# Kernel optimization log

Measured on AMD Instinct MI355X. Metric: run time of the kernel, lower is better.

The kernel has to match this reference:

```python
import jax, jax.numpy as jnp
import numpy as np

N, D, HID, E, XD = 50000, 128, 64, 800000, 3

def _p(key, shape, scale=0.05):
    return jax.random.normal(key, shape, dtype=jnp.float32) * scale

def setup_inputs() -> dict:
    key = jax.random.key(0)
    ks = jax.random.split(key, 16)
    h = jax.random.normal(ks[0], (N, D), dtype=jnp.float32)
    x = jax.random.normal(ks[1], (N, XD), dtype=jnp.float32)
    edge_index = jax.random.randint(ks[2], (2, E), 0, N, dtype=jnp.int32)
    return {
        'h': h, 'x': x, 'edge_index': edge_index,
        'We1': _p(ks[3], (HID, 2 * D + 1)), 'be1': jnp.zeros((HID,), jnp.float32),
        'We2': _p(ks[4], (HID, HID)), 'be2': jnp.zeros((HID,), jnp.float32),
        'ln_g': jnp.ones((HID,), jnp.float32), 'ln_b': jnp.zeros((HID,), jnp.float32),
        'Wh1': _p(ks[5], (HID, D + HID)), 'bh1': jnp.zeros((HID,), jnp.float32),
        'Wh2': _p(ks[6], (D, HID)), 'bh2': jnp.zeros((D,), jnp.float32),
        'Wx': _p(ks[7], (1, HID)), 'bx': jnp.zeros((1,), jnp.float32),
        'Wg': _p(ks[8], (1, HID)), 'bg': jnp.zeros((1,), jnp.float32),
    }

def reference(h, x, edge_index, We1, be1, We2, be2, ln_g, ln_b,
              Wh1, bh1, Wh2, bh2, Wx, bx, Wg, bg):
    src, dst = edge_index[0], edge_index[1]
    n_nodes = h.shape[0]
    r = x[src] - x[dst]                          # (E, 3)
    d_sq = jnp.sum(r * r, axis=-1, keepdims=True)  # (E, 1)
    r_n = r / (jnp.sqrt(d_sq) + 1e-8)
    # phi_e: Linear -> SiLU -> Linear -> SiLU -> LayerNorm
    e_in = jnp.concatenate([h[src], h[dst], d_sq], axis=-1)  # (E, 2d+1)
    z = jax.nn.silu(e_in @ We1.T + be1)
    z = jax.nn.silu(z @ We2.T + be2)
    mu = jnp.mean(z, axis=-1, keepdims=True)
    var = jnp.mean((z - mu) ** 2, axis=-1, keepdims=True)
    m = (z - mu) * jax.lax.rsqrt(var + 1e-5) * ln_g + ln_b   # (E, hid)
    # gate and gated messages
    alpha = jax.nn.sigmoid(m @ Wg.T + bg)                     # (E, 1)
    m_gated = m * alpha
    agg_h = jax.ops.segment_sum(m_gated, dst, num_segments=n_nodes)  # (N, hid)
    # coordinate update (tanh_coords=True)
    cw = jnp.tanh(m_gated @ Wx.T + bx)                        # (E, 1)
    agg_x = jax.ops.segment_sum(r_n * cw, dst, num_segments=n_nodes)  # (N, 3)
    # coords_agg='mean': divide by in-degree clamped to 1
    deg = jax.ops.segment_sum(jnp.ones((src.shape[0], 1), h.dtype), dst,
                              num_segments=n_nodes)
    agg_x = agg_x / jnp.maximum(deg, 1.0)
    # phi_h residual update
    hh = jax.nn.silu(jnp.concatenate([h, agg_h], axis=-1) @ Wh1.T + bh1)
    h_new = h + (hh @ Wh2.T + bh2)
    x_new = x + agg_x
    return (h_new, x_new)
```

## Files before the change

### kernel.cpp

```cpp
#include <hip/hip_runtime.h>
#include <math.h>

#define HID 64
#define DF  128
#define HB  256

typedef __attribute__((ext_vector_type(8))) short short8v;
typedef __attribute__((ext_vector_type(4))) float float4v;
typedef __attribute__((ext_vector_type(4))) unsigned int uint4v;

__device__ __forceinline__ float silu_f(float v) {
    return v * __builtin_amdgcn_rcpf(1.0f + __expf(-v));
}

__device__ __forceinline__ unsigned short f2bf(float f) {
    unsigned u = __float_as_uint(f);
    u += 0x7FFFu + ((u >> 16) & 1u);
    return (unsigned short)(u >> 16);
}

__device__ __forceinline__ unsigned cvt2(float lo, float hi) {
    unsigned r;
    asm("v_cvt_pk_bf16_f32 %0, %1, %2" : "=v"(r) : "v"(lo), "v"(hi));
    return r;
}

__device__ __forceinline__ short8v pack8(float a0, float a1, float a2, float a3,
                                         float a4, float a5, float a6, float a7) {
    uint4v w;
    w[0] = cvt2(a0, a1);
    w[1] = cvt2(a2, a3);
    w[2] = cvt2(a4, a5);
    w[3] = cvt2(a6, a7);
    union { uint4v u; short8v s; } cv;
    cv.u = w;
    return cv.s;
}

__device__ __forceinline__ short8v pack_bf16(float4 a, float4 b) {
    return pack8(a.x, a.y, a.z, a.w, b.x, b.y, b.z, b.w);
}

__device__ __forceinline__ void wredsum4(float& a, float& b, float& c, float& d) {
#pragma unroll
    for (int t = 1; t < 64; t <<= 1) {
        a += __shfl_xor(a, t, 64);
        b += __shfl_xor(b, t, 64);
        c += __shfl_xor(c, t, 64);
        d += __shfl_xor(d, t, 64);
    }
}

#define PREPW 61504
__global__ void prep_weights(const float* __restrict__ We1, const float* __restrict__ We2,
                             const float* __restrict__ Wh1, const float* __restrict__ Wh2,
                             float* __restrict__ Wt1, float* __restrict__ Wt2,
                             unsigned short* __restrict__ WbfA,
                             unsigned short* __restrict__ WpB1,
                             unsigned short* __restrict__ WpH1,
                             unsigned short* __restrict__ WpH2,
                             int* __restrict__ cnt, int N) {
    int i = blockIdx.x * 256 + threadIdx.x;
    if (i >= PREPW) {
        int n = i - PREPW;
        if (n < N) cnt[n] = 0;
        return;
    }
    if (i < 257 * 64) {
        int k = i >> 6, f = i & 63;
        Wt1[i] = We1[f * 257 + k];
        return;
    }
    int j = i - 257 * 64;
    if (j < 64 * 64) {
        int k = j >> 6, f = j & 63;
        Wt2[j] = We2[f * 64 + k];
        return;
    }
    j -= 64 * 64;
    if (j < 4096) {
        int jj = j & 7, lane = (j >> 3) & 63, kc = (j >> 9) & 1, t = (j >> 10) & 3;
        int f = t * 16 + (lane & 15);
        int k = kc * 32 + ((lane >> 4) * 8) + jj;
        WbfA[j] = f2bf(We2[f * 64 + k]);
        return;
    }
    j -= 4096;
    if (j < 16384) {
        int jj = j & 7, lane = (j >> 3) & 63, kc = (j >> 9) & 3, ft = j >> 11;
        int f = ft * 16 + (lane & 15);
        int k = kc * 32 + ((lane >> 4) * 8) + jj;
        float v = (f < 64) ? We1[f * 257 + k] : We1[(f - 64) * 257 + 128 + k];
        WpB1[j] = f2bf(v);
        return;
    }
    j -= 16384;
    if (j < 12288) {
        int jj = j & 7, lane = (j >> 3) & 63, idx = j >> 9;
        int kc = idx % 6, ft = idx / 6;
        int f = ft * 16 + (lane & 15);
        int k = kc * 32 + ((lane >> 4) * 8) + jj;
        WpH1[j] = f2bf(Wh1[f * 192 + k]);
        return;
    }
    j -= 12288;
    if (j < 8192) {
        int jj = j & 7, lane = (j >> 3) & 63, idx = j >> 9;
        int kc = idx & 1, ft = idx >> 1;
        int c = ft * 16 + (lane & 15);
        int k = kc * 32 + ((lane >> 4) * 8) + jj;
        WpH2[j] = f2bf(Wh2[c * 64 + k]);
        return;
    }
}

__global__ __launch_bounds__(256) void count_kernel(const int* __restrict__ dst,
                                                    int* __restrict__ cnt,
                                                    int* __restrict__ rank, int E) {
    int e = blockIdx.x * 256 + threadIdx.x;
    if (e >= E) return;
    int r = atomicAdd(&cnt[dst[e]], 1);
    if (rank) rank[e] = r;
}

__global__ __launch_bounds__(1024) void scan1(const int* __restrict__ cnt,
                                              int* __restrict__ off,
                                              int* __restrict__ bsum, int N) {
    __shared__ int sm[1024];
    int tid = threadIdx.x;
    int i = blockIdx.x * 1024 + tid;
    int v = (i < N) ? cnt[i] : 0;
    sm[tid] = v;
    __syncthreads();
    for (int ofs = 1; ofs < 1024; ofs <<= 1) {
        int t = (tid >= ofs) ? sm[tid - ofs] : 0;
        __syncthreads();
        sm[tid] += t;
        __syncthreads();
    }
    if (i < N) off[i] = sm[tid] - v;
    if (tid == 1023) bsum[blockIdx.x] = sm[1023];
}

__global__ __launch_bounds__(256) void scan3(int* __restrict__ off,
                                             const int* __restrict__ bsum,
                                             int Nb, int N, int E) {
    __shared__ int pref[64];
    if (threadIdx.x == 0) {
        int s = 0;
        for (int b = 0; b < Nb; ++b) { pref[b] = s; s += bsum[b]; }
    }
    __syncthreads();
    int i = blockIdx.x * 256 + threadIdx.x;
    if (i > N) return;
    if (i == N) off[N] = E;
    else off[i] += pref[i >> 10];
}

__global__ __launch_bounds__(256) void scatter_src(const int* __restrict__ dst,
                                                   const int* __restrict__ srcI,
                                                   const int* __restrict__ rank,
                                                   const int* __restrict__ off,
                                                   int* __restrict__ csr_src, int E) {
    int e = blockIdx.x * 256 + threadIdx.x;
    if (e >= E) return;
    csr_src[off[dst[e]] + rank[e]] = srcI[e];
}

__global__ __launch_bounds__(HB) void hist_local(const int* __restrict__ cnt,
                                                 int* __restrict__ lrank,
                                                 int* __restrict__ blockcnt, int N) {
    __shared__ int lh[64];
    int tid = threadIdx.x;
    if (tid < 64) lh[tid] = 0;
    __syncthreads();
    int n = blockIdx.x * HB + tid;
    if (n < N) {
        int b = min(cnt[n], 63);
        lrank[n] = atomicAdd(&lh[b], 1);
    }
    __syncthreads();
    if (tid < 64) blockcnt[blockIdx.x * 64 + tid] = lh[tid];
}

__global__ __launch_bounds__(1024) void hist_tot(const int* __restrict__ blockcnt,
                                                 int* __restrict__ bucketbase, int nblk) {
    __shared__ int part[16][64];
    int b = threadIdx.x & 63, j = threadIdx.x >> 6;
    int s = 0;
    for (int k = j; k < nblk; k += 16) s += blockcnt[k * 64 + b];
    part[j][b] = s;
    __syncthreads();
    if (threadIdx.x < 64) {
        int t = 0;
#pragma unroll
        for (int jj = 1; jj < 16; ++jj) t += part[jj][threadIdx.x];
        part[0][threadIdx.x] += t;
    }
    __syncthreads();
    if (threadIdx.x == 0) {
        int base = 0;
        for (int bb = 0; bb < 64; ++bb) {
            int t = part[0][bb];
            bucketbase[bb] = base;
            base += t;
        }
    }
}

__global__ __launch_bounds__(64) void hist_scan2(int* __restrict__ blockcnt,
                                                 const int* __restrict__ bucketbase,
                                                 int nblk) {
    int b = blockIdx.x;
    int lane = threadIdx.x;
    int carry = bucketbase[b];
    for (int chunk = 0; chunk * 64 < nblk; ++chunk) {
        int k = chunk * 64 + lane;
        int c = (k < nblk) ? blockcnt[k * 64 + b] : 0;
        int v = c;
#pragma unroll
        for (int ofs = 1; ofs < 64; ofs <<= 1) {
            int t = __shfl_up(v, ofs, 64);
            if (lane >= ofs) v += t;
        }
        if (k < nblk) blockcnt[k * 64 + b] = carry + v - c;
        carry += __shfl(v, 63, 64);
    }
}

__global__ __launch_bounds__(HB) void degscatter2(const int* __restrict__ cnt,
                                                  const int* __restrict__ lrank,
                                                  const int* __restrict__ blockcnt,
                                                  int* __restrict__ nodeorder, int N) {
    int n = blockIdx.x * HB + threadIdx.x;
    if (n >= N) return;
    int b = min(cnt[n], 63);
    int pos = blockcnt[(n / HB) * 64 + b] + lrank[n];
    nodeorder[N - 1 - pos] = n;
}

__global__ __launch_bounds__(256) void node_pre(
    const float* __restrict__ h, const unsigned short* __restrict__ WpB1,
    const float* __restrict__ be1, const float* __restrict__ xin,
    float* __restrict__ Ps, float* __restrict__ Pd,
    float4* __restrict__ x4, int N) {
    const int lane = threadIdx.x & 63;
    const int wslot = threadIdx.x >> 6;
    {
        int n = blockIdx.x * 64 + threadIdx.x;
        if (threadIdx.x < 64 && n < N)
            x4[n] = make_float4(xin[3 * n], xin[3 * n + 1], xin[3 * n + 2], 0.f);
    }
    const int tile = (blockIdx.x * 4 + wslot) * 16;
    if (tile >= N) return;
    const int r15 = lane & 15, kg = lane >> 4;
    const int arow = min(tile + r15, N - 1);
    const float* hr = h + (size_t)arow * DF + kg * 8;
    short8v A[4];
#pragma unroll
    for (int kc = 0; kc < 4; ++kc) {
        float4 q0 = *(const float4*)(hr + kc * 32);
        float4 q1 = *(const float4*)(hr + kc * 32 + 4);
        A[kc] = pack_bf16(q0, q1);
    }
#pragma unroll
    for (int ft = 0; ft < 8; ++ft) {
        float4v c = (float4v){0.f, 0.f, 0.f, 0.f};
#pragma unroll
        for (int kc = 0; kc < 4; ++kc) {
            short8v B = *(const short8v*)&WpB1[(((ft * 4 + kc) * 64) + lane) * 8];
            c = __builtin_amdgcn_mfma_f32_16x16x32_bf16(A[kc], B, c, 0, 0, 0);
        }
        int f = ft * 16 + r15;
        float bias = (f >= 64) ? be1[f - 64] : 0.f;
#pragma unroll
        for (int r = 0; r < 4; ++r) {
            int n = tile + kg * 4 + r;
            if (n < N) {
                float v = c[r] + bias;
                if (f < 64) Ps[(size_t)n * 64 + f] = v;
                else        Pd[(size_t)n * 64 + (f - 64)] = v;
            }
        }
    }
}

__global__ __launch_bounds__(256) void gather_kernel(
    const int* __restrict__ csr_src, const int* __restrict__ off,
    const int* __restrict__ nodeorder, const float4* __restrict__ x4,
    const float* __restrict__ Ps, const float* __restrict__ Pd,
    const float* __restrict__ Wt1, const unsigned short* __restrict__ WbfA,
    const float* __restrict__ be2,
    const float* __restrict__ ln_g, const float* __restrict__ ln_b,
    const float* __restrict__ Wx, const float* __restrict__ bx,
    const float* __restrict__ Wg, const float* __restrict__ bg,
    float* __restrict__ agg_h, float* __restrict__ xout, int N) {
    const int lane = threadIdx.x & 63;
    const int wid = blockIdx.x * 4 + (threadIdx.x >> 6);
    const int e16 = lane & 15;
    const int hg = lane >> 4;
    const int k0 = hg * 8;
    const int p = e16 & 3;
    if (wid * 4 >= N) return;
    const int slot = wid * 4 + (e16 >> 2);

    short8v a[4][2];
#pragma unroll
    for (int t = 0; t < 4; ++t)
#pragma unroll
        for (int kc = 0; kc < 2; ++kc)
            a[t][kc] = *(const short8v*)&WbfA[(((t * 2 + kc) * 64) + lane) * 8];

    const float* colW = Wt1 + 256 * HID;
    float colWk[16];
#pragma unroll
    for (int j = 0; j < 8; ++j) {
        colWk[j] = colW[k0 + j];
        colWk[8 + j] = colW[k0 + 32 + j];
    }
    float be2r[16], cgr[16], cxr[16];
#pragma unroll
    for (int t = 0; t < 4; ++t)
#pragma unroll
        for (int r = 0; r < 4; ++r) {
            int f = t * 16 + hg * 4 + r;
            float g = ln_g[f];
            be2r[4 * t + r] = be2[f];
            cgr[4 * t + r] = g * Wg[f];
            cxr[4 * t + r] = g * Wx[f];
        }
    const float bgs = bg[0], bxs = bx[0];

    float Cg = ln_g[lane] * Wg[lane], Cx = ln_g[lane] * Wx[lane];
    float Cbg = ln_b[lane] * Wg[lane], Cbx = ln_b[lane] * Wx[lane];
    wredsum4(Cg, Cx, Cbg, Cbx);
    const float g0 = (lane < 16) ? 1.0f : 0.0f;

    const int nj = (slot < N) ? nodeorder[slot] : -1;
    int beg = 0, end = 0;
    if (nj >= 0) { beg = off[nj]; end = off[nj + 1]; }
    const float4 xdv = (nj >= 0) ? x4[nj] : make_float4(0.f, 0.f, 0.f, 0.f);
    float baseK[16];
    {
        const float4v* pd4 = (const float4v*)(Pd + (size_t)max(nj, 0) * HID + k0);
        float4v p0 = pd4[0], p1 = pd4[1], p2 = pd4[8], p3 = pd4[9];
#pragma unroll
        for (int j = 0; j < 4; ++j) {
            baseK[j] = p0[j];
            baseK[4 + j] = p1[j];
            baseK[8 + j] = p2[j];
            baseK[12 + j] = p3[j];
        }
    }

    int nb = (end - beg + 3) >> 2;
#pragma unroll
    for (int mk = 1; mk < 64; mk <<= 1) nb = max(nb, __shfl_xor(nb, mk, 64));
    nb = __builtin_amdgcn_readfirstlane(nb);

    float4v acc[4];
#pragma unroll
    for (int t = 0; t < 4; ++t) acc[t] = (float4v){0.f, 0.f, 0.f, 0.f};
    float ax0 = 0.f, ax1 = 0.f, ax2 = 0.f, Sa = 0.f, Smu = 0.f;

    float4 xsC = xdv;
    float4v q0C = (float4v){0.f, 0.f, 0.f, 0.f}, q1C = q0C, q2C = q0C, q3C = q0C;
    if (nb > 0) {
        int idx = beg + p;
        int ic = (idx < end) ? idx : (end > 0 ? end - 1 : 0);
        int s0 = csr_src[ic];
        xsC = x4[s0];
        const float4v* ps4 = (const float4v*)(Ps + (size_t)s0 * HID + k0);
        q0C = ps4[0]; q1C = ps4[1]; q2C = ps4[8]; q3C = ps4[9];
    }

    for (int b = 0; b < nb; ++b) {
        float4 xs = xsC;
        float4v q0 = q0C, q1 = q1C, q2 = q2C, q3 = q3C;
        float validf = ((beg + b * 4 + p) < end) ? 1.0f : 0.0f;

        if (b + 1 < nb) {
            int idx2 = beg + (b + 1) * 4 + p;
            int ic2 = (idx2 < end) ? idx2 : (end > 0 ? end - 1 : 0);
            int sN = csr_src[ic2];
            xsC = x4[sN];
            const float4v* ps4 = (const float4v*)(Ps + (size_t)sN * HID + k0);
            q0C = ps4[0]; q1C = ps4[1]; q2C = ps4[8]; q3C = ps4[9];
        }

        float r0 = xs.x - xdv.x, r1 = xs.y - xdv.y, r2 = xs.z - xdv.z;
        float dsq = r0 * r0 + r1 * r1 + r2 * r2;
        float inv = __builtin_amdgcn_rcpf(__builtin_amdgcn_sqrtf(dsq) + 1e-8f);

        float zb[16];
#pragma unroll
        for (int j = 0; j < 4; ++j) {
            zb[j]      = silu_f(q0[j] + baseK[j] + dsq * colWk[j]);
            zb[4 + j]  = silu_f(q1[j] + baseK[4 + j] + dsq * colWk[4 + j]);
            zb[8 + j]  = silu_f(q2[j] + baseK[8 + j] + dsq * colWk[8 + j]);
            zb[12 + j] = silu_f(q3[j] + baseK[12 + j] + dsq * colWk[12 + j]);
        }
        short8v b0 = pack8(zb[0], zb[1], zb[2], zb[3], zb[4], zb[5], zb[6], zb[7]);
        short8v b1 = pack8(zb[8], zb[9], zb[10], zb[11], zb[12], zb[13], zb[14], zb[15]);

        float ms[16];
        float S1 = 0.f, S2 = 0.f, Sg = 0.f, Sx = 0.f;
#pragma unroll
        for (int t = 0; t < 4; ++t) {
            float4v c = (float4v){be2r[4 * t], be2r[4 * t + 1],
                                  be2r[4 * t + 2], be2r[4 * t + 3]};
            c = __builtin_amdgcn_mfma_f32_16x16x32_bf16(a[t][0], b0, c, 0, 0, 0);
            c = __builtin_amdgcn_mfma_f32_16x16x32_bf16(a[t][1], b1, c, 0, 0, 0);
#pragma unroll
            for (int r = 0; r < 4; ++r) {
                float v = c[r] * __builtin_amdgcn_rcpf(1.0f + __expf(-c[r]));
                ms[4 * t + r] = v;
                S1 += v;
                S2 = fmaf(v, v, S2);
                Sg = fmaf(v, cgr[4 * t + r], Sg);
                Sx = fmaf(v, cxr[4 * t + r], Sx);
            }
        }
#pragma unroll
        for (int mk = 16; mk < 64; mk <<= 1) {
            S1 += __shfl_xor(S1, mk, 64);
            S2 += __shfl_xor(S2, mk, 64);
            Sg += __shfl_xor(Sg, mk, 64);
            Sx += __shfl_xor(Sx, mk, 64);
        }

        float mu = S1 * (1.0f / HID);
        float var = S2 * (1.0f / HID) - mu * mu;
        float rstd = __builtin_amdgcn_rsqf(var + 1e-5f);
        float dg = fmaf(rstd, Sg - mu * Cg, Cbg);
        float dx = fmaf(rstd, Sx - mu * Cx, Cbx);
        float alpha = __builtin_amdgcn_rcpf(1.0f + __expf(-(dg + bgs))) * validf;
        float ta = __expf(2.0f * fmaf(alpha, dx, bxs));
        float cwv = 1.0f - 2.0f * __builtin_amdgcn_rcpf(ta + 1.0f);

        float u = rstd * alpha;
        Sa += alpha;
        Smu = fmaf(u, mu, Smu);
#pragma unroll
        for (int t = 0; t < 4; ++t) {
            float4v av = acc[t];
#pragma unroll
            for (int r = 0; r < 4; ++r) av[r] = fmaf(u, ms[4 * t + r], av[r]);
            acc[t] = av;
        }
        float rc = inv * cwv * validf * g0;
        ax0 = fmaf(r0, rc, ax0);
        ax1 = fmaf(r1, rc, ax1);
        ax2 = fmaf(r2, rc, ax2);
    }

#pragma unroll
    for (int t = 0; t < 4; ++t) {
        float4v av = acc[t];
#pragma unroll
        for (int r = 0; r < 4; ++r) {
            float v = av[r];
            v += __shfl_xor(v, 1, 64);
            v += __shfl_xor(v, 2, 64);
            av[r] = v;
        }
        acc[t] = av;
    }
    Sa  += __shfl_xor(Sa, 1, 64);  Sa  += __shfl_xor(Sa, 2, 64);
    Smu += __shfl_xor(Smu, 1, 64); Smu += __shfl_xor(Smu, 2, 64);
    ax0 += __shfl_xor(ax0, 1, 64); ax0 += __shfl_xor(ax0, 2, 64);
    ax1 += __shfl_xor(ax1, 1, 64); ax1 += __shfl_xor(ax1, 2, 64);
    ax2 += __shfl_xor(ax2, 1, 64); ax2 += __shfl_xor(ax2, 2, 64);

    if (p == 0 && nj >= 0) {
        float* dstp = agg_h + (size_t)nj * HID + hg * 4;
#pragma unroll
        for (int t = 0; t < 4; ++t) {
            int f = t * 16 + hg * 4;
            float4 o;
            o.x = fmaf(ln_g[f + 0], acc[t][0] - Smu, ln_b[f + 0] * Sa);
            o.y = fmaf(ln_g[f + 1], acc[t][1] - Smu, ln_b[f + 1] * Sa);
            o.z = fmaf(ln_g[f + 2], acc[t][2] - Smu, ln_b[f + 2] * Sa);
            o.w = fmaf(ln_g[f + 3], acc[t][3] - Smu, ln_b[f + 3] * Sa);
            *(float4*)(dstp + t * 16) = o;
        }
        if (hg == 0) {
            float invd = 1.0f / fmaxf((float)(end - beg), 1.0f);
            float* ox = xout + (size_t)nj * 3;
            ox[0] = xdv.x + ax0 * invd;
            ox[1] = xdv.y + ax1 * invd;
            ox[2] = xdv.z + ax2 * invd;
        }
    }
}

__global__ __launch_bounds__(256) void edge_kernel_atomic(
    const int* __restrict__ src, const int* __restrict__ dst,
    const float* __restrict__ x,
    const float* __restrict__ Ps, const float* __restrict__ Pd,
    const float* __restrict__ Wt1, const float* __restrict__ Wt2,
    const float* __restrict__ be2,
    const float* __restrict__ ln_g, const float* __restrict__ ln_b,
    const float* __restrict__ Wx, const float* __restrict__ bx,
    const float* __restrict__ Wg, const float* __restrict__ bg,
    float* __restrict__ agg_h, float* __restrict__ agg_x, int E) {
    int e = blockIdx.x * 256 + threadIdx.x;
    if (e >= E) return;
    int s = src[e], d = dst[e];
    float r0 = x[s * 3] - x[d * 3], r1 = x[s * 3 + 1] - x[d * 3 + 1], r2 = x[s * 3 + 2] - x[d * 3 + 2];
    float dsq = r0 * r0 + r1 * r1 + r2 * r2;
    float inv = 1.0f / (sqrtf(dsq) + 1e-8f);
    float rn0 = r0 * inv, rn1 = r1 * inv, rn2 = r2 * inv;
    float z[HID];
    const float4* ps = (const float4*)(Ps + (size_t)s * HID);
    const float4* pd = (const float4*)(Pd + (size_t)d * HID);
    const float* colW = Wt1 + 256 * HID;
#pragma unroll
    for (int f4 = 0; f4 < HID / 4; ++f4) {
        float4 aa = ps[f4];
        float4 b = pd[f4];
        float av[4] = {aa.x, aa.y, aa.z, aa.w};
        float bv[4] = {b.x, b.y, b.z, b.w};
#pragma unroll
        for (int j = 0; j < 4; ++j) {
            int f = 4 * f4 + j;
            z[f] = silu_f(av[j] + bv[j] + dsq * colW[f]);
        }
    }
    float m[HID];
#pragma unroll
    for (int f = 0; f < HID; ++f) m[f] = be2[f];
#pragma unroll
    for (int k = 0; k < HID; ++k) {
        float zv = z[k];
#pragma unroll
        for (int f = 0; f < HID; ++f) m[f] = fmaf(zv, Wt2[k * HID + f], m[f]);
    }
#pragma unroll
    for (int f = 0; f < HID; ++f) m[f] = silu_f(m[f]);
    float mu = 0.f;
#pragma unroll
    for (int f = 0; f < HID; ++f) mu += m[f];
    mu *= (1.0f / HID);
    float var = 0.f;
#pragma unroll
    for (int f = 0; f < HID; ++f) {
        float t = m[f] - mu;
        var = fmaf(t, t, var);
    }
    var *= (1.0f / HID);
    float rstd = 1.0f / sqrtf(var + 1e-5f);
#pragma unroll
    for (int f = 0; f < HID; ++f) m[f] = (m[f] - mu) * rstd * ln_g[f] + ln_b[f];
    float dotg = 0.f, dotx = 0.f;
#pragma unroll
    for (int f = 0; f < HID; ++f) {
        dotg = fmaf(m[f], Wg[f], dotg);
        dotx = fmaf(m[f], Wx[f], dotx);
    }
    float alpha = 1.0f / (1.0f + __expf(-(dotg + bg[0])));
    float ta = __expf(2.0f * fmaf(alpha, dotx, bx[0]));
    float cw = 1.0f - 2.0f / (ta + 1.0f);
    float* ah = agg_h + (size_t)d * HID;
#pragma unroll
    for (int f = 0; f < HID; ++f) atomicAdd(&ah[f], m[f] * alpha);
    atomicAdd(&agg_x[d * 3 + 0], rn0 * cw);
    atomicAdd(&agg_x[d * 3 + 1], rn1 * cw);
    atomicAdd(&agg_x[d * 3 + 2], rn2 * cw);
}

__global__ __launch_bounds__(256) void node_kernel(
    const float* __restrict__ h, const float* __restrict__ xin,
    const float* __restrict__ agg_h, const float* __restrict__ agg_x,
    const int* __restrict__ degI,
    const unsigned short* __restrict__ WpH1, const unsigned short* __restrict__ WpH2,
    const float* __restrict__ bh1, const float* __restrict__ bh2,
    float* __restrict__ out, int N, int writeX) {
    __shared__ float hhL[4][16][72];
    const int lane = threadIdx.x & 63;
    const int wslot = threadIdx.x >> 6;
    if (writeX) {
        int n = blockIdx.x * 64 + threadIdx.x;
        if (threadIdx.x < 64 && n < N) {
            float dv = (float)degI[n];
            float invd = 1.0f / fmaxf(dv, 1.0f);
            float* ox = out + (size_t)N * DF + (size_t)n * 3;
            ox[0] = xin[n * 3 + 0] + agg_x[n * 3 + 0] * invd;
            ox[1] = xin[n * 3 + 1] + agg_x[n * 3 + 1] * invd;
            ox[2] = xin[n * 3 + 2] + agg_x[n * 3 + 2] * invd;
        }
    }
    const int tile = (blockIdx.x * 4 + wslot) * 16;
    if (tile >= N) return;
    const int r15 = lane & 15, kg = lane >> 4;
    const int arow = min(tile + r15, N - 1);

    short8v A[6];
    const float* hr = h + (size_t)arow * DF + kg * 8;
#pragma unroll
    for (int kc = 0; kc < 4; ++kc) {
        float4 q0 = *(const float4*)(hr + kc * 32);
        float4 q1 = *(const float4*)(hr + kc * 32 + 4);
        A[kc] = pack_bf16(q0, q1);
    }
    const float* ar = agg_h + (size_t)arow * HID + kg * 8;
#pragma unroll
    for (int kc = 0; kc < 2; ++kc) {
        float4 q0 = *(const float4*)(ar + kc * 32);
        float4 q1 = *(const float4*)(ar + kc * 32 + 4);
        A[4 + kc] = pack_bf16(q0, q1);
    }

#pragma unroll
    for (int ft = 0; ft < 4; ++ft) {
        float4v c = (float4v){0.f, 0.f, 0.f, 0.f};
#pragma unroll
        for (int kc = 0; kc < 6; ++kc) {
            short8v B = *(const short8v*)&WpH1[(((ft * 6 + kc) * 64) + lane) * 8];
            c = __builtin_amdgcn_mfma_f32_16x16x32_bf16(A[kc], B, c, 0, 0, 0);
        }
        int f = ft * 16 + r15;
        float b1v = bh1[f];
#pragma unroll
        for (int r = 0; r < 4; ++r)
            hhL[wslot][kg * 4 + r][f] = silu_f(c[r] + b1v);
    }
    __builtin_amdgcn_wave_barrier();

    short8v HA[2];
#pragma unroll
    for (int kc = 0; kc < 2; ++kc) {
        float4 q0 = *(const float4*)&hhL[wslot][r15][kc * 32 + kg * 8];
        float4 q1 = *(const float4*)&hhL[wslot][r15][kc * 32 + kg * 8 + 4];
        HA[kc] = pack_bf16(q0, q1);
    }

#pragma unroll
    for (int ft = 0; ft < 8; ++ft) {
        float4v c = (float4v){0.f, 0.f, 0.f, 0.f};
#pragma unroll
        for (int kc = 0; kc < 2; ++kc) {
            short8v B = *(const short8v*)&WpH2[(((ft * 2 + kc) * 64) + lane) * 8];
            c = __builtin_amdgcn_mfma_f32_16x16x32_bf16(HA[kc], B, c, 0, 0, 0);
        }
        int cc = ft * 16 + r15;
        float b2 = bh2[cc];
#pragma unroll
        for (int r = 0; r < 4; ++r) {
            int n = tile + kg * 4 + r;
            if (n < N)
                out[(size_t)n * DF + cc] = h[(size_t)n * DF + cc] + c[r] + b2;
        }
    }
}

extern "C" void kernel_launch(void* const* d_in, const int* in_sizes, int n_in,
                              void* d_out, int out_size, void* d_ws, size_t ws_size,
                              hipStream_t stream) {
    const float* h    = (const float*)d_in[0];
    const float* x    = (const float*)d_in[1];
    const int*   ei   = (const int*)d_in[2];
    const float* We1  = (const float*)d_in[3];
    const float* be1  = (const float*)d_in[4];
    const float* We2  = (const float*)d_in[5];
    const float* be2  = (const float*)d_in[6];
    const float* ln_g = (const float*)d_in[7];
    const float* ln_b = (const float*)d_in[8];
    const float* Wh1  = (const float*)d_in[9];
    const float* bh1  = (const float*)d_in[10];
    const float* Wh2  = (const float*)d_in[11];
    const float* bh2  = (const float*)d_in[12];
    const float* Wx   = (const float*)d_in[13];
    const float* bx   = (const float*)d_in[14];
    const float* Wg   = (const float*)d_in[15];
    const float* bg   = (const float*)d_in[16];

    const int E = in_sizes[2] / 2;
    const int N = in_sizes[0] / DF;
    const int* src = ei;
    const int* dst = ei + E;

    char* base = (char*)d_ws;
    size_t o = 0;
    auto carve = [&](size_t bytes) -> void* {
        void* r = base + o;
        o = (o + bytes + 15) & ~(size_t)15;
        return r;
    };
    const int nblk = (N + HB - 1) / HB;
    float* agg_h = (float*)carve((size_t)N * HID * 4);
    float* agg_x = (float*)carve((size_t)N * 3 * 4);
    float* Wt1   = (float*)carve(257 * 64 * 4);
    float* Wt2   = (float*)carve(64 * 64 * 4);
    unsigned short* WbfA = (unsigned short*)carve(4096 * 2);
    unsigned short* WpB1 = (unsigned short*)carve(16384 * 2);
    unsigned short* WpH1 = (unsigned short*)carve(12288 * 2);
    unsigned short* WpH2 = (unsigned short*)carve(8192 * 2);
    int*   cnt   = (int*)carve((size_t)N * 4);
    int*   off   = (int*)carve(((size_t)N + 1) * 4);
    int*   bsum  = (int*)carve(256 * 4);
    int*   lrank = (int*)carve((size_t)N * 4);
    int*   blockcnt = (int*)carve((size_t)nblk * 64 * 4);
    int*   bucketbase = (int*)carve(64 * 4);
    int*   nodeorder = (int*)carve((size_t)N * 4);
    float4* x4   = (float4*)carve((size_t)N * 16);
    int*   rank  = (int*)carve((size_t)E * 4);
    int*   csr_src = (int*)carve((size_t)E * 4);
    size_t need_full = o;

    float* Ps = (float*)d_out;
    float* Pd = Ps + (size_t)N * HID;
    float* xout = (float*)d_out + (size_t)N * DF;

    const int gE  = (E + 255) / 256;
    const int Nb  = (N + 1023) / 1024;
    const int tiles = (N + 15) / 16;
    const int gT  = (tiles + 3) / 4;

    prep_weights<<<(PREPW + N + 255) / 256, 256, 0, stream>>>(
        We1, We2, Wh1, Wh2, Wt1, Wt2, WbfA, WpB1, WpH1, WpH2, cnt, N);
    node_pre<<<gT, 256, 0, stream>>>(h, WpB1, be1, x, Ps, Pd, x4, N);

    if (ws_size >= need_full) {
        count_kernel<<<gE, 256, 0, stream>>>(dst, cnt, rank, E);
        scan1<<<Nb, 1024, 0, stream>>>(cnt, off, bsum, N);
        scan3<<<(N + 256) / 256, 256, 0, stream>>>(off, bsum, Nb, N, E);
        scatter_src<<<gE, 256, 0, stream>>>(dst, src, rank, off, csr_src, E);
        hist_local<<<nblk, HB, 0, stream>>>(cnt, lrank, blockcnt, N);
        hist_tot<<<1, 1024, 0, stream>>>(blockcnt, bucketbase, nblk);
        hist_scan2<<<64, 64, 0, stream>>>(blockcnt, bucketbase, nblk);
        degscatter2<<<nblk, HB, 0, stream>>>(cnt, lrank, blockcnt, nodeorder, N);
        const int quads = (N + 3) / 4;
        gather_kernel<<<(quads + 3) / 4, 256, 0, stream>>>(
            csr_src, off, nodeorder, x4, Ps, Pd, Wt1, WbfA, be2,
            ln_g, ln_b, Wx, bx, Wg, bg, agg_h, xout, N);
        node_kernel<<<gT, 256, 0, stream>>>(h, x, agg_h, agg_x, cnt,
                                            WpH1, WpH2, bh1, bh2, (float*)d_out, N, 0);
    } else {
        hipMemsetAsync(agg_h, 0, (size_t)N * 67 * 4, stream);
        count_kernel<<<gE, 256, 0, stream>>>(dst, cnt, nullptr, E);
        edge_kernel_atomic<<<gE, 256, 0, stream>>>(src, dst, x, Ps, Pd, Wt1, Wt2,
                                                   be2, ln_g, ln_b, Wx, bx,
                                                   Wg, bg, agg_h, agg_x, E);
        node_kernel<<<gT, 256, 0, stream>>>(h, x, agg_h, agg_x, cnt,
                                            WpH1, WpH2, bh1, bh2, (float*)d_out, N, 1);
    }
}
```

Baseline: 185.9 us.

## Merge degree histogram scan kernels and load LN-gate coefficients from memory

Replaces the hist_tot and hist_scan2 pair with a single hist_scan3 kernel. Each 64-thread block redundantly sums the bucket totals, scans them, and writes block offsets to a separate buffer, which removes one launch and its serialization. The gather kernel no longer keeps 48 per-lane registers of be2 and ln_g-scaled Wg/Wx. It loads them as float4s from precomputed cgL/cxL arrays inside the loop, with an opaque zero offset so the compiler cannot hoist them back into registers. This is meant to lower register pressure and raise occupancy, at the cost of extra cached loads on every iteration.

```diff
diff --git a/kernel.cpp b/kernel.cpp
--- a/kernel.cpp
+++ b/kernel.cpp
@@ -51,14 +51,17 @@
     }
 }
 
-#define PREPW 61504
+#define PREPW 61632
 __global__ void prep_weights(const float* __restrict__ We1, const float* __restrict__ We2,
                              const float* __restrict__ Wh1, const float* __restrict__ Wh2,
+                             const float* __restrict__ ln_g,
+                             const float* __restrict__ Wg, const float* __restrict__ Wx,
                              float* __restrict__ Wt1, float* __restrict__ Wt2,
                              unsigned short* __restrict__ WbfA,
                              unsigned short* __restrict__ WpB1,
                              unsigned short* __restrict__ WpH1,
                              unsigned short* __restrict__ WpH2,
+                             float* __restrict__ cgL, float* __restrict__ cxL,
                              int* __restrict__ cnt, int N) {
     int i = blockIdx.x * 256 + threadIdx.x;
     if (i >= PREPW) {
@@ -110,6 +113,16 @@
         int c = ft * 16 + (lane & 15);
         int k = kc * 32 + ((lane >> 4) * 8) + jj;
         WpH2[j] = f2bf(Wh2[c * 64 + k]);
+        return;
+    }
+    j -= 8192;
+    if (j < 64) {
+        cgL[j] = ln_g[j] * Wg[j];
+        return;
+    }
+    j -= 64;
+    if (j < 64) {
+        cxL[j] = ln_g[j] * Wx[j];
         return;
     }
 }
@@ -183,59 +196,42 @@
     if (tid < 64) blockcnt[blockIdx.x * 64 + tid] = lh[tid];
 }
 
-__global__ __launch_bounds__(1024) void hist_tot(const int* __restrict__ blockcnt,
-                                                 int* __restrict__ bucketbase, int nblk) {
-    __shared__ int part[16][64];
-    int b = threadIdx.x & 63, j = threadIdx.x >> 6;
+__global__ __launch_bounds__(64) void hist_scan3(const int* __restrict__ blockcnt,
+                                                 int* __restrict__ blockoff, int nblk) {
+    const int b = blockIdx.x;
+    const int lane = threadIdx.x;
     int s = 0;
-    for (int k = j; k < nblk; k += 16) s += blockcnt[k * 64 + b];
-    part[j][b] = s;
-    __syncthreads();
-    if (threadIdx.x < 64) {
-        int t = 0;
-#pragma unroll
-        for (int jj = 1; jj < 16; ++jj) t += part[jj][threadIdx.x];
-        part[0][threadIdx.x] += t;
-    }
-    __syncthreads();
-    if (threadIdx.x == 0) {
-        int base = 0;
-        for (int bb = 0; bb < 64; ++bb) {
-            int t = part[0][bb];
-            bucketbase[bb] = base;
-            base += t;
-        }
-    }
-}
-
-__global__ __launch_bounds__(64) void hist_scan2(int* __restrict__ blockcnt,
-                                                 const int* __restrict__ bucketbase,
-                                                 int nblk) {
-    int b = blockIdx.x;
-    int lane = threadIdx.x;
-    int carry = bucketbase[b];
+    for (int k = 0; k < nblk; ++k) s += blockcnt[k * 64 + lane];
+    int v = s;
+#pragma unroll
+    for (int ofs = 1; ofs < 64; ofs <<= 1) {
+        int t = __shfl_up(v, ofs, 64);
+        if (lane >= ofs) v += t;
+    }
+    int base_b = __shfl(v - s, b, 64);
+    int carry = base_b;
     for (int chunk = 0; chunk * 64 < nblk; ++chunk) {
         int k = chunk * 64 + lane;
         int c = (k < nblk) ? blockcnt[k * 64 + b] : 0;
-        int v = c;
+        int w = c;
 #pragma unroll
         for (int ofs = 1; ofs < 64; ofs <<= 1) {
-            int t = __shfl_up(v, ofs, 64);
-            if (lane >= ofs) v += t;
-        }
-        if (k < nblk) blockcnt[k * 64 + b] = carry + v - c;
-        carry += __shfl(v, 63, 64);
+            int t = __shfl_up(w, ofs, 64);
+            if (lane >= ofs) w += t;
+        }
+        if (k < nblk) blockoff[k * 64 + b] = carry + w - c;
+        carry += __shfl(w, 63, 64);
     }
 }
 
 __global__ __launch_bounds__(HB) void degscatter2(const int* __restrict__ cnt,
                                                   const int* __restrict__ lrank,
-                                                  const int* __restrict__ blockcnt,
+                                                  const int* __restrict__ blockoff,
                                                   int* __restrict__ nodeorder, int N) {
     int n = blockIdx.x * HB + threadIdx.x;
     if (n >= N) return;
     int b = min(cnt[n], 63);
-    int pos = blockcnt[(n / HB) * 64 + b] + lrank[n];
+    int pos = blockoff[(n / HB) * 64 + b] + lrank[n];
     nodeorder[N - 1 - pos] = n;
 }
 
@@ -291,9 +287,10 @@
     const float* __restrict__ Ps, const float* __restrict__ Pd,
     const float* __restrict__ Wt1, const unsigned short* __restrict__ WbfA,
     const float* __restrict__ be2,
+    const float* __restrict__ cgL, const float* __restrict__ cxL,
     const float* __restrict__ ln_g, const float* __restrict__ ln_b,
-    const float* __restrict__ Wx, const float* __restrict__ bx,
-    const float* __restrict__ Wg, const float* __restrict__ bg,
+    const float* __restrict__ bx, const float* __restrict__ bg,
+    const float* __restrict__ Wg, const float* __restrict__ Wx,
     float* __restrict__ agg_h, float* __restrict__ xout, int N) {
     const int lane = threadIdx.x & 63;
     const int wid = blockIdx.x * 4 + (threadIdx.x >> 6);
@@ -318,17 +315,6 @@
         colWk[j] = colW[k0 + j];
         colWk[8 + j] = colW[k0 + 32 + j];
     }
-    float be2r[16], cgr[16], cxr[16];
-#pragma unroll
-    for (int t = 0; t < 4; ++t)
-#pragma unroll
-        for (int r = 0; r < 4; ++r) {
-            int f = t * 16 + hg * 4 + r;
-            float g = ln_g[f];
-            be2r[4 * t + r] = be2[f];
-            cgr[4 * t + r] = g * Wg[f];
-            cxr[4 * t + r] = g * Wx[f];
-        }
     const float bgs = bg[0], bxs = bx[0];
 
     float Cg = ln_g[lane] * Wg[lane], Cx = ln_g[lane] * Wx[lane];
@@ -403,22 +389,32 @@
         short8v b0 = pack8(zb[0], zb[1], zb[2], zb[3], zb[4], zb[5], zb[6], zb[7]);
         short8v b1 = pack8(zb[8], zb[9], zb[10], zb[11], zb[12], zb[13], zb[14], zb[15]);
 
+        int zz;
+        asm volatile("v_mov_b32 %0, 0" : "=v"(zz));
+        const float* be2b = be2 + zz;
+        const float* cgb = cgL + zz;
+        const float* cxb = cxL + zz;
+
         float ms[16];
         float S1 = 0.f, S2 = 0.f, Sg = 0.f, Sx = 0.f;
 #pragma unroll
         for (int t = 0; t < 4; ++t) {
-            float4v c = (float4v){be2r[4 * t], be2r[4 * t + 1],
-                                  be2r[4 * t + 2], be2r[4 * t + 3]};
+            float4 b2v = *(const float4*)&be2b[t * 16 + hg * 4];
+            float4 cgv = *(const float4*)&cgb[t * 16 + hg * 4];
+            float4 cxv = *(const float4*)&cxb[t * 16 + hg * 4];
+            float4v c = (float4v){b2v.x, b2v.y, b2v.z, b2v.w};
             c = __builtin_amdgcn_mfma_f32_16x16x32_bf16(a[t][0], b0, c, 0, 0, 0);
             c = __builtin_amdgcn_mfma_f32_16x16x32_bf16(a[t][1], b1, c, 0, 0, 0);
+            float cg4[4] = {cgv.x, cgv.y, cgv.z, cgv.w};
+            float cx4[4] = {cxv.x, cxv.y, cxv.z, cxv.w};
 #pragma unroll
             for (int r = 0; r < 4; ++r) {
                 float v = c[r] * __builtin_amdgcn_rcpf(1.0f + __expf(-c[r]));
                 ms[4 * t + r] = v;
                 S1 += v;
                 S2 = fmaf(v, v, S2);
-                Sg = fmaf(v, cgr[4 * t + r], Sg);
-                Sx = fmaf(v, cxr[4 * t + r], Sx);
+                Sg = fmaf(v, cg4[r], Sg);
+                Sx = fmaf(v, cx4[r], Sx);
             }
         }
 #pragma unroll
@@ -696,12 +692,14 @@
     unsigned short* WpB1 = (unsigned short*)carve(16384 * 2);
     unsigned short* WpH1 = (unsigned short*)carve(12288 * 2);
     unsigned short* WpH2 = (unsigned short*)carve(8192 * 2);
+    float* cgL   = (float*)carve(64 * 4);
+    float* cxL   = (float*)carve(64 * 4);
     int*   cnt   = (int*)carve((size_t)N * 4);
     int*   off   = (int*)carve(((size_t)N + 1) * 4);
     int*   bsum  = (int*)carve(256 * 4);
     int*   lrank = (int*)carve((size_t)N * 4);
     int*   blockcnt = (int*)carve((size_t)nblk * 64 * 4);
-    int*   bucketbase = (int*)carve(64 * 4);
+    int*   blockoff = (int*)carve((size_t)nblk * 64 * 4);
     int*   nodeorder = (int*)carve((size_t)N * 4);
     float4* x4   = (float4*)carve((size_t)N * 16);
     int*   rank  = (int*)carve((size_t)E * 4);
@@ -718,7 +716,8 @@
     const int gT  = (tiles + 3) / 4;
 
     prep_weights<<<(PREPW + N + 255) / 256, 256, 0, stream>>>(
-        We1, We2, Wh1, Wh2, Wt1, Wt2, WbfA, WpB1, WpH1, WpH2, cnt, N);
+        We1, We2, Wh1, Wh2, ln_g, Wg, Wx,
+        Wt1, Wt2, WbfA, WpB1, WpH1, WpH2, cgL, cxL, cnt, N);
     node_pre<<<gT, 256, 0, stream>>>(h, WpB1, be1, x, Ps, Pd, x4, N);
 
     if (ws_size >= need_full) {
@@ -727,13 +726,12 @@
         scan3<<<(N + 256) / 256, 256, 0, stream>>>(off, bsum, Nb, N, E);
         scatter_src<<<gE, 256, 0, stream>>>(dst, src, rank, off, csr_src, E);
         hist_local<<<nblk, HB, 0, stream>>>(cnt, lrank, blockcnt, N);
-        hist_tot<<<1, 1024, 0, stream>>>(blockcnt, bucketbase, nblk);
-        hist_scan2<<<64, 64, 0, stream>>>(blockcnt, bucketbase, nblk);
-        degscatter2<<<nblk, HB, 0, stream>>>(cnt, lrank, blockcnt, nodeorder, N);
+        hist_scan3<<<64, 64, 0, stream>>>(blockcnt, blockoff, nblk);
+        degscatter2<<<nblk, HB, 0, stream>>>(cnt, lrank, blockoff, nodeorder, N);
         const int quads = (N + 3) / 4;
         gather_kernel<<<(quads + 3) / 4, 256, 0, stream>>>(
             csr_src, off, nodeorder, x4, Ps, Pd, Wt1, WbfA, be2,
-            ln_g, ln_b, Wx, bx, Wg, bg, agg_h, xout, N);
+            cgL, cxL, ln_g, ln_b, bx, bg, Wg, Wx, agg_h, xout, N);
         node_kernel<<<gT, 256, 0, stream>>>(h, x, agg_h, agg_x, cnt,
                                             WpH1, WpH2, bh1, bh2, (float*)d_out, N, 0);
     } else {
```

Measured after the change: 215.6 us. 16.0% more time.
